# Optimization experiments

Measured on AMD Instinct MI355X. Metric: run time of the kernel, lower is better.

Reference implementation:

```python
import jax, jax.numpy as jnp
import numpy as np

B, P, H, N, D, K = 1024, 1024, 4096, 32, 512, 128


def setup_inputs() -> dict:
    key = jax.random.key(0)
    k1, k2, k3, k4, k5 = jax.random.split(key, 5)
    return {
        "proximal_input": jax.random.normal(k1, (B, P), dtype=jnp.float32),
        "distal_input": jax.random.normal(k2, (B, D), dtype=jnp.float32),
        "W": jax.random.normal(k3, (H, P), dtype=jnp.float32) / np.sqrt(P),
        "b": jax.random.normal(k4, (H,), dtype=jnp.float32) / np.sqrt(P),
        "distal": jax.random.normal(k5, (H, N, D), dtype=jnp.float32),
        "k": K,
    }


def reference(proximal_input, distal_input, W, b, distal, k):
    # proximal path: standard linear -> (B, H)
    proximal_output = proximal_input @ W.T + b
    # per-hidden-unit dendrite projections -> (H, B, N)
    distal_output = jnp.einsum('bd,hnd->hbn', distal_input, distal)
    # pick dominant dendrite by absolute value, keep its signed value
    abs_max_idx = jnp.argmax(jnp.abs(distal_output), axis=-1)          # (H, B)
    distal_max = jnp.take_along_axis(
        distal_output, abs_max_idx[..., None], axis=-1)[..., 0].T      # (B, H)
    # sigmoid gate modulates proximal activations
    result = proximal_output * jax.nn.sigmoid(distal_max)              # (B, H)
    # keep only top-k per row (scatter-built 0/1 mask, as in the original)
    _, top_idxs = jax.lax.top_k(result, k)                             # (B, k)
    rows = jnp.arange(result.shape[0])[:, None]
    mask = jnp.zeros_like(result).at[rows, top_idxs].set(1.0)
    return result * mask
```

## Files before the change

### kernel.cpp

```cpp
#include <hip/hip_runtime.h>
#include <cstdint>
#include <cmath>

#define Bsz  1024
#define Pdim 1024
#define Hdim 4096
#define Ndim 32
#define Ddim 512
#define Ktop 128

typedef _Float16 f16x8  __attribute__((ext_vector_type(8)));
typedef float    f32x16 __attribute__((ext_vector_type(16)));

#define GLDS(gsrc, ldst)                                                        \
  __builtin_amdgcn_global_load_lds(                                             \
      (const __attribute__((address_space(1))) unsigned int*)(gsrc),            \
      (__attribute__((address_space(3))) unsigned int*)(ldst), 16, 0, 0)

#define WS_SERIAL 270532608ull
#define OFF_DIN   268435456ull
#define OFF_W     270532608ull
#define OFF_PIN   287309824ull
#define OFF_GATE  291504128ull
#define WS_FUSED  308281344ull

__global__ __launch_bounds__(256) void convert_img(
    const float* __restrict__ src, char* __restrict__ dst, int kcbits)
{
  const int gid  = blockIdx.x * 256 + threadIdx.x;
  const int row  = gid >> kcbits;
  const int e    = (gid & ((1 << kcbits) - 1)) * 8;
  const int Krow = 8 << kcbits;
  float4 v0 = *(const float4*)(src + (size_t)row * Krow + e);
  float4 v1 = *(const float4*)(src + (size_t)row * Krow + e + 4);
  const int tile = row >> 7, r = row & 127, ks = e >> 5, k = e & 31;
  char* base = dst + (size_t)(tile * (Krow >> 5) + ks) * 16384;
  const int off = ((r >> 5) * 2 + (k >> 4)) * 1024
                + ((r & 31) + 32 * ((k >> 3) & 1)) * 16;
  const float f[8] = {v0.x, v0.y, v0.z, v0.w, v1.x, v1.y, v1.z, v1.w};
  f16x8 hi, lo;
#pragma unroll
  for (int j = 0; j < 8; j++) {
    const _Float16 h = (_Float16)f[j];
    hi[j] = h;
    lo[j] = (_Float16)((f[j] - (float)h) * 256.f);
  }
  *(f16x8*)(base + off)        = hi;
  *(f16x8*)(base + 8192 + off) = lo;
}

template <int NH>
__device__ __forceinline__ void pipe_gemm(
    char (*lds)[16384], const char* Abase, const char* Bbase,
    int lane16, int wv, int wr, int wc,
    f32x16 acc[2][2], f32x16 accx[2][2])
{
  auto STAGE = [&](int h) {
    const int ks = h >> 1, kk = h & 1;
    char* buf = lds[h & 3];
    const char* Ai = Abase + (size_t)ks * 16384;
    const char* Bi = Bbase + (size_t)ks * 16384;
    const char* srcs[4] = {Ai, Ai + 8192, Bi, Bi + 8192};
#pragma unroll
    for (int j = 0; j < 4; j++) {
      const int c = j * 4 + wv;
      GLDS(srcs[j] + (wv * 2 + kk) * 1024 + lane16, buf + c * 1024);
    }
  };

  STAGE(0);
  STAGE(1);
  asm volatile("s_waitcnt vmcnt(4)" ::: "memory");
  __builtin_amdgcn_s_barrier();
  __builtin_amdgcn_sched_barrier(0);

  for (int h = 0; h < NH; ++h) {
    const char* buf = lds[h & 3];
    f16x8 ah[2], al[2], bh[2], bl[2];
#pragma unroll
    for (int mi = 0; mi < 2; mi++) {
      const int m = wr * 2 + mi;
      ah[mi] = *(const f16x8*)(buf + m * 1024 + lane16);
      al[mi] = *(const f16x8*)(buf + 4096 + m * 1024 + lane16);
    }
#pragma unroll
    for (int ni = 0; ni < 2; ni++) {
      const int m = wc * 2 + ni;
      bh[ni] = *(const f16x8*)(buf + 8192 + m * 1024 + lane16);
      bl[ni] = *(const f16x8*)(buf + 12288 + m * 1024 + lane16);
    }
    __builtin_amdgcn_sched_barrier(0);
    if (h + 2 < NH) STAGE(h + 2);
    __builtin_amdgcn_s_barrier();
    __builtin_amdgcn_sched_barrier(0);
    __builtin_amdgcn_s_setprio(1);
#pragma unroll
    for (int ni = 0; ni < 2; ni++)
#pragma unroll
      for (int mi = 0; mi < 2; mi++) {
        acc[mi][ni]  = __builtin_amdgcn_mfma_f32_32x32x16_f16(ah[mi], bh[ni], acc[mi][ni],  0, 0, 0);
        accx[mi][ni] = __builtin_amdgcn_mfma_f32_32x32x16_f16(ah[mi], bl[ni], accx[mi][ni], 0, 0, 0);
        accx[mi][ni] = __builtin_amdgcn_mfma_f32_32x32x16_f16(al[mi], bh[ni], accx[mi][ni], 0, 0, 0);
      }
    __builtin_amdgcn_s_setprio(0);
    if (h + 2 < NH) {
      asm volatile("s_waitcnt vmcnt(4)" ::: "memory");
    } else if (h + 1 < NH) {
      asm volatile("s_waitcnt vmcnt(0)" ::: "memory");
    }
    if (h + 1 < NH) {
      __builtin_amdgcn_s_barrier();
      __builtin_amdgcn_sched_barrier(0);
    }
  }
}

__device__ __forceinline__ void epi_prox(
    f32x16 acc[2][2], f32x16 accx[2][2], const float* bias, float* out,
    int h0, int b0, int wr, int wc, int hi32, int c31)
{
#pragma unroll
  for (int mi = 0; mi < 2; ++mi)
#pragma unroll
    for (int ni = 0; ni < 2; ++ni) {
      const int bcol = b0 + wc * 64 + ni * 32 + c31;
#pragma unroll
      for (int qq = 0; qq < 4; ++qq) {
        const int hb = h0 + wr * 64 + mi * 32 + qq * 8 + hi32 * 4;
        const float4 bb = *(const float4*)(bias + hb);
        float4 o;
        o.x = acc[mi][ni][4*qq+0] + accx[mi][ni][4*qq+0] * 0.00390625f + bb.x;
        o.y = acc[mi][ni][4*qq+1] + accx[mi][ni][4*qq+1] * 0.00390625f + bb.y;
        o.z = acc[mi][ni][4*qq+2] + accx[mi][ni][4*qq+2] * 0.00390625f + bb.z;
        o.w = acc[mi][ni][4*qq+3] + accx[mi][ni][4*qq+3] * 0.00390625f + bb.w;
        *(float4*)(out + (size_t)bcol * Hdim + hb) = o;
      }
    }
}

__device__ __forceinline__ void epi_distal(
    f32x16 acc[2][2], f32x16 accx[2][2], float* out, float* gates,
    int ntile, int btile, int wr, int wc, int hi32, int c31)
{
#pragma unroll
  for (int mi = 0; mi < 2; ++mi)
#pragma unroll
    for (int ni = 0; ni < 2; ++ni) {
      float bestA = -1.f, bestV = 0.f;
      int   bestN = 999;
#pragma unroll
      for (int reg = 0; reg < 16; ++reg) {
        const float v = acc[mi][ni][reg] + accx[mi][ni][reg] * 0.00390625f;
        const float a = fabsf(v);
        const int   n = (reg & 3) + 8 * (reg >> 2) + 4 * hi32;
        if (a > bestA) { bestA = a; bestV = v; bestN = n; }
      }
      {
        const float oa = __shfl_xor(bestA, 32, 64);
        const float ov = __shfl_xor(bestV, 32, 64);
        const int   on = __shfl_xor(bestN, 32, 64);
        if (oa > bestA || (oa == bestA && on < bestN)) {
          bestA = oa; bestV = ov; bestN = on;
        }
      }
      if (hi32 == 0) {
        const int bcol = btile * 128 + wc * 64 + ni * 32 + c31;
        const int h    = ntile * 4 + wr * 2 + mi;
        const float gate = 1.f / (1.f + expf(-bestV));
        const size_t idx = (size_t)bcol * Hdim + h;
        if (gates) gates[idx] = gate;
        else       out[idx] *= gate;
      }
    }
}

__global__ __launch_bounds__(256, 2) void fused_mfma(
    const char* __restrict__ Wimg, const char* __restrict__ Pimg,
    const float* __restrict__ bias, float* __restrict__ out,
    const char* __restrict__ Dimg, const char* __restrict__ Nimg,
    float* __restrict__ gates)
{
  __shared__ __align__(16) char lds[4][16384];
  const int t = threadIdx.x, lane = t & 63, wv = t >> 6;
  const int lane16 = lane * 16;
  const int hi32 = lane >> 5, c31 = lane & 31;
  const int wr = wv >> 1, wc = wv & 1;

  f32x16 acc[2][2], accx[2][2];
#pragma unroll
  for (int mi = 0; mi < 2; mi++)
#pragma unroll
    for (int ni = 0; ni < 2; ni++) {
      acc[mi][ni]  = (f32x16)(0.f);
      accx[mi][ni] = (f32x16)(0.f);
    }

  if (blockIdx.x < 256) {
    const int blk = blockIdx.x;
    const int xcd = blk & 7, q = blk >> 3;
    const int htile = xcd * 4 + (q >> 3);
    const int btile = q & 7;
    pipe_gemm<64>(lds, Wimg + (size_t)(htile * 32) * 16384,
                  Pimg + (size_t)(btile * 32) * 16384,
                  lane16, wv, wr, wc, acc, accx);
    epi_prox(acc, accx, bias, out, htile * 128, btile * 128, wr, wc, hi32, c31);
  } else {
    const int blk = blockIdx.x - 256;
    const int xcd = blk & 7, q = blk >> 3;
    const int ntile = xcd * 128 + (q >> 3);
    const int btile = q & 7;
    pipe_gemm<32>(lds, Dimg + (size_t)(ntile * 16) * 16384,
                  Nimg + (size_t)(btile * 16) * 16384,
                  lane16, wv, wr, wc, acc, accx);
    epi_distal(acc, accx, out, gates, ntile, btile, wr, wc, hi32, c31);
  }
}

__global__ __launch_bounds__(256, 2) void proximal_mfma(
    const char* __restrict__ Aw, const char* __restrict__ Bw,
    const float* __restrict__ bias, float* __restrict__ out)
{
  __shared__ __align__(16) char lds[4][16384];
  const int t = threadIdx.x, lane = t & 63, wv = t >> 6;
  const int lane16 = lane * 16;
  const int hi32 = lane >> 5, c31 = lane & 31;
  const int wr = wv >> 1, wc = wv & 1;
  const int blk = blockIdx.x;
  const int xcd = blk & 7, q = blk >> 3;
  const int htile = xcd * 4 + (q >> 3);
  const int btile = q & 7;

  f32x16 acc[2][2], accx[2][2];
#pragma unroll
  for (int mi = 0; mi < 2; mi++)
#pragma unroll
    for (int ni = 0; ni < 2; ni++) {
      acc[mi][ni]  = (f32x16)(0.f);
      accx[mi][ni] = (f32x16)(0.f);
    }
  pipe_gemm<64>(lds, Aw + (size_t)(htile * 32) * 16384,
                Bw + (size_t)(btile * 32) * 16384,
                lane16, wv, wr, wc, acc, accx);
  epi_prox(acc, accx, bias, out, htile * 128, btile * 128, wr, wc, hi32, c31);
}

__global__ __launch_bounds__(256, 2) void distal_mfma(
    const char* __restrict__ Aw, const char* __restrict__ Bw,
    float* __restrict__ out)
{
  __shared__ __align__(16) char lds[4][16384];
  const int t = threadIdx.x, lane = t & 63, wv = t >> 6;
  const int lane16 = lane * 16;
  const int hi32 = lane >> 5, c31 = lane & 31;
  const int wr = wv >> 1, wc = wv & 1;
  const int blk = blockIdx.x;
  const int xcd = blk & 7, q = blk >> 3;
  const int ntile = xcd * 128 + (q >> 3);
  const int btile = q & 7;

  f32x16 acc[2][2], accx[2][2];
#pragma unroll
  for (int mi = 0; mi < 2; mi++)
#pragma unroll
    for (int ni = 0; ni < 2; ni++) {
      acc[mi][ni]  = (f32x16)(0.f);
      accx[mi][ni] = (f32x16)(0.f);
    }
  pipe_gemm<32>(lds, Aw + (size_t)(ntile * 16) * 16384,
                Bw + (size_t)(btile * 16) * 16384,
                lane16, wv, wr, wc, acc, accx);
  epi_distal(acc, accx, out, nullptr, ntile, btile, wr, wc, hi32, c31);
}

__global__ __launch_bounds__(256) void proximal_gemm(
    const float* __restrict__ pin, const float* __restrict__ W,
    const float* __restrict__ bias, float* __restrict__ out)
{
  __shared__ float Blds[32 * 256];
  __shared__ float Alds[32 * 32];
  const int t  = threadIdx.x;
  const int l  = t & 63;
  const int wv = t >> 6;
  const int ell   = blockIdx.x;
  const int xcd   = ell & 7;
  const int q     = ell >> 3;
  const int htile = xcd * 2 + (q >> 5);
  const int btile = q & 31;
  const int h0 = htile * 256, b0 = btile * 32;

  float acc[8][4];
#pragma unroll
  for (int i = 0; i < 8; i++)
    for (int j = 0; j < 4; j++) acc[i][j] = 0.f;

  const float* wrow = W + (size_t)(h0 + t) * Pdim;
  const int ab = t >> 3, ak = (t & 7) * 4;
  const float* arow = pin + (size_t)(b0 + ab) * Pdim + ak;

  for (int kt = 0; kt < Pdim / 32; ++kt) {
    const int p0 = kt * 32;
    float wbuf[32];
#pragma unroll
    for (int f = 0; f < 8; f++) {
      float4 v = *(const float4*)(wrow + p0 + f * 4);
      wbuf[f * 4 + 0] = v.x; wbuf[f * 4 + 1] = v.y;
      wbuf[f * 4 + 2] = v.z; wbuf[f * 4 + 3] = v.w;
    }
    float4 av = *(const float4*)(arow + p0);
    __syncthreads();
#pragma unroll
    for (int f = 0; f < 32; f++) Blds[f * 256 + t] = wbuf[f];
    Alds[(ak + 0) * 32 + ab] = av.x;
    Alds[(ak + 1) * 32 + ab] = av.y;
    Alds[(ak + 2) * 32 + ab] = av.z;
    Alds[(ak + 3) * 32 + ab] = av.w;
    __syncthreads();
#pragma unroll
    for (int k = 0; k < 32; k++) {
      float4 bv  = *(const float4*)&Blds[k * 256 + 4 * l];
      float4 alo = *(const float4*)&Alds[k * 32 + 8 * wv];
      float4 ahi = *(const float4*)&Alds[k * 32 + 8 * wv + 4];
      float a0[8] = {alo.x, alo.y, alo.z, alo.w, ahi.x, ahi.y, ahi.z, ahi.w};
#pragma unroll
      for (int i = 0; i < 8; i++) {
        acc[i][0] += a0[i] * bv.x;
        acc[i][1] += a0[i] * bv.y;
        acc[i][2] += a0[i] * bv.z;
        acc[i][3] += a0[i] * bv.w;
      }
    }
  }
  float4 bb = *(const float4*)(bias + h0 + 4 * l);
#pragma unroll
  for (int i = 0; i < 8; i++) {
    float4 o;
    o.x = acc[i][0] + bb.x;
    o.y = acc[i][1] + bb.y;
    o.z = acc[i][2] + bb.z;
    o.w = acc[i][3] + bb.w;
    *(float4*)(out + (size_t)(b0 + 8 * wv + i) * Hdim + h0 + 4 * l) = o;
  }
}

__global__ __launch_bounds__(256) void distal_gate_fb(
    const float* __restrict__ din, const float* __restrict__ distal,
    float* __restrict__ out)
{
  __shared__ float Blds[32 * 256];
  __shared__ float Alds[32 * 32];
  const int t  = threadIdx.x;
  const int l  = t & 63;
  const int wv = t >> 6;
  const int ell   = blockIdx.x;
  const int xcd   = ell & 7;
  const int q     = ell >> 3;
  const int htile = xcd * 64 + (q >> 5);
  const int btile = q & 31;
  const int n0 = htile * 256, b0 = btile * 32;

  float acc[8][4];
#pragma unroll
  for (int i = 0; i < 8; i++)
    for (int j = 0; j < 4; j++) acc[i][j] = 0.f;

  const float* brow = distal + (size_t)(n0 + t) * Ddim;
  const int ab = t >> 3, ak = (t & 7) * 4;
  const float* arow = din + (size_t)(b0 + ab) * Ddim + ak;

  for (int kt = 0; kt < Ddim / 32; ++kt) {
    const int d0 = kt * 32;
    float wbuf[32];
#pragma unroll
    for (int f = 0; f < 8; f++) {
      float4 v = *(const float4*)(brow + d0 + f * 4);
      wbuf[f * 4 + 0] = v.x; wbuf[f * 4 + 1] = v.y;
      wbuf[f * 4 + 2] = v.z; wbuf[f * 4 + 3] = v.w;
    }
    float4 av = *(const float4*)(arow + d0);
    __syncthreads();
#pragma unroll
    for (int f = 0; f < 32; f++) Blds[f * 256 + t] = wbuf[f];
    Alds[(ak + 0) * 32 + ab] = av.x;
    Alds[(ak + 1) * 32 + ab] = av.y;
    Alds[(ak + 2) * 32 + ab] = av.z;
    Alds[(ak + 3) * 32 + ab] = av.w;
    __syncthreads();
#pragma unroll
    for (int k = 0; k < 32; k++) {
      float4 bv  = *(const float4*)&Blds[k * 256 + 4 * l];
      float4 alo = *(const float4*)&Alds[k * 32 + 8 * wv];
      float4 ahi = *(const float4*)&Alds[k * 32 + 8 * wv + 4];
      float a0[8] = {alo.x, alo.y, alo.z, alo.w, ahi.x, ahi.y, ahi.z, ahi.w};
#pragma unroll
      for (int i = 0; i < 8; i++) {
        acc[i][0] += a0[i] * bv.x;
        acc[i][1] += a0[i] * bv.y;
        acc[i][2] += a0[i] * bv.z;
        acc[i][3] += a0[i] * bv.w;
      }
    }
  }
  const int i0  = l & 7;
  const int grp = l >> 3;
  float v = 0.f;
#pragma unroll
  for (int bi = 0; bi < 8; bi++) {
    float bav = fabsf(acc[bi][0]);
    float bv_ = acc[bi][0];
    int   bn  = 4 * i0;
#pragma unroll
    for (int j = 1; j < 4; j++) {
      float av2 = fabsf(acc[bi][j]);
      if (av2 > bav) { bav = av2; bv_ = acc[bi][j]; bn = 4 * i0 + j; }
    }
#pragma unroll
    for (int m = 1; m < 8; m <<= 1) {
      float oav = __shfl_xor(bav, m, 64);
      float ov  = __shfl_xor(bv_, m, 64);
      int   on  = __shfl_xor(bn,  m, 64);
      if (oav > bav || (oav == bav && on < bn)) { bav = oav; bv_ = ov; bn = on; }
    }
    if (bi == i0) v = bv_;
  }
  const float gate = 1.f / (1.f + expf(-v));
  const size_t idx = (size_t)(b0 + 8 * wv + i0) * Hdim + (size_t)htile * 8 + grp;
  out[idx] *= gate;
}

__device__ __forceinline__ unsigned keyf(float f) {
  unsigned u = __float_as_uint(f);
  return (u & 0x80000000u) ? ~u : (u | 0x80000000u);
}

__global__ __launch_bounds__(256) void topk_mask(
    float* __restrict__ out, const float* __restrict__ gates)
{
  __shared__ float vals[Hdim];
  __shared__ unsigned hist[256];
  __shared__ unsigned sc[4];
  __shared__ unsigned s_prefix, s_kk;
  const int t = threadIdx.x;
  float* row = out + (size_t)blockIdx.x * Hdim;
  const float* grow = gates ? gates + (size_t)blockIdx.x * Hdim : nullptr;

#pragma unroll
  for (int qq = 0; qq < 4; qq++) {
    float4 v = *(const float4*)(row + qq * 1024 + t * 4);
    if (grow) {
      float4 g = *(const float4*)(grow + qq * 1024 + t * 4);
      v.x *= g.x; v.y *= g.y; v.z *= g.z; v.w *= g.w;
    }
    *(float4*)&vals[qq * 1024 + t * 4] = v;
  }
  if (t == 0) { s_prefix = 0u; s_kk = Ktop; }
  __syncthreads();

  for (int shift = 24; shift >= 0; shift -= 8) {
    hist[t] = 0u;
    __syncthreads();
    const unsigned prefix = s_prefix;
    const unsigned maskhi = (shift == 24) ? 0u : (0xFFFFFFFFu << (shift + 8));
    for (int c = 0; c < 16; c++) {
      unsigned u = keyf(vals[c * 256 + t]);
      if ((u & maskhi) == prefix)
        atomicAdd(&hist[(u >> shift) & 255u], 1u);
    }
    __syncthreads();
    if (t == 0) {
      unsigned kk = s_kk, cum = 0;
      int bin = 255;
      for (; bin > 0; --bin) {
        unsigned c = hist[bin];
        if (cum + c >= kk) break;
        cum += c;
      }
      s_kk = kk - cum;
      s_prefix = prefix | ((unsigned)bin << shift);
    }
    __syncthreads();
  }
  const unsigned T  = s_prefix;
  const unsigned kk = s_kk;

  const int lane = t & 63, w = t >> 6;
  unsigned running = 0;
  for (int c = 0; c < 16; c++) {
    const int h = c * 256 + t;
    const float v = vals[h];
    const unsigned u = keyf(v);
    const bool tie = (u == T);
    unsigned long long m = __ballot(tie);
    unsigned lpfx = (unsigned)__popcll(m & ((1ull << lane) - 1ull));
    if (lane == 0) sc[w] = (unsigned)__popcll(m);
    __syncthreads();
    unsigned off = 0;
#pragma unroll
    for (int ww = 0; ww < 4; ww++) if (ww < w) off += sc[ww];
    const unsigned rank = running + off + lpfx;
    row[h] = (u > T) ? v : ((tie && rank < kk) ? v : 0.f);
    const unsigned tot = sc[0] + sc[1] + sc[2] + sc[3];
    __syncthreads();
    running += tot;
  }
}

extern "C" void kernel_launch(void* const* d_in, const int* in_sizes, int n_in,
                              void* d_out, int out_size, void* d_ws, size_t ws_size,
                              hipStream_t stream)
{
  (void)in_sizes; (void)n_in; (void)out_size;
  const float* pin  = (const float*)d_in[0];
  const float* dinp = (const float*)d_in[1];
  const float* W    = (const float*)d_in[2];
  const float* bias = (const float*)d_in[3];
  const float* dst  = (const float*)d_in[4];
  float* out = (float*)d_out;

  char* ws = (char*)d_ws;
  if (ws_size >= WS_FUSED) {
    hipLaunchKernelGGL(convert_img, dim3(32768), dim3(256), 0, stream, dst,  ws,            6);
    hipLaunchKernelGGL(convert_img, dim3(256),   dim3(256), 0, stream, dinp, ws + OFF_DIN,  6);
    hipLaunchKernelGGL(convert_img, dim3(2048),  dim3(256), 0, stream, W,    ws + OFF_W,    7);
    hipLaunchKernelGGL(convert_img, dim3(512),   dim3(256), 0, stream, pin,  ws + OFF_PIN,  7);
    hipLaunchKernelGGL(fused_mfma,  dim3(8448),  dim3(256), 0, stream,
                       ws + OFF_W, ws + OFF_PIN, bias, out,
                       ws, ws + OFF_DIN, (float*)(ws + OFF_GATE));
    hipLaunchKernelGGL(topk_mask,   dim3(Bsz),   dim3(256), 0, stream, out,
                       (const float*)(ws + OFF_GATE));
  } else if (ws_size >= WS_SERIAL) {
    hipLaunchKernelGGL(convert_img,   dim3(2048),  dim3(256), 0, stream, W,   ws,            7);
    hipLaunchKernelGGL(convert_img,   dim3(512),   dim3(256), 0, stream, pin, ws + 16777216, 7);
    hipLaunchKernelGGL(proximal_mfma, dim3(256),   dim3(256), 0, stream, ws, ws + 16777216, bias, out);
    hipLaunchKernelGGL(convert_img,   dim3(32768), dim3(256), 0, stream, dst,  ws,           6);
    hipLaunchKernelGGL(convert_img,   dim3(256),   dim3(256), 0, stream, dinp, ws + OFF_DIN, 6);
    hipLaunchKernelGGL(distal_mfma,   dim3(8192),  dim3(256), 0, stream, ws, ws + OFF_DIN, out);
    hipLaunchKernelGGL(topk_mask,     dim3(Bsz),   dim3(256), 0, stream, out, (const float*)nullptr);
  } else {
    hipLaunchKernelGGL(proximal_gemm,  dim3(512),   dim3(256), 0, stream, pin, W, bias, out);
    hipLaunchKernelGGL(distal_gate_fb, dim3(16384), dim3(256), 0, stream, dinp, dst, out);
    hipLaunchKernelGGL(topk_mask,      dim3(Bsz),   dim3(256), 0, stream, out, (const float*)nullptr);
  }
}
```

Baseline: 601.7 us.

## Double-buffer MFMA fragments in registers and deepen LDS prefetch to three stages

Restructures the GEMM main loop so the LDS fragments for step h+1 are read into a second register set while MFMAs for step h run. Global-to-LDS prefetch distance grows from two to three stages within the 4-slot ring. It also drops one barrier per iteration. The aim is to hide LDS read latency and global load latency behind the matrix ops, at the cost of more VGPRs and a possible ring-slot hazard, since the stage for h+3 is issued before the reads of h+1 have been fenced by a barrier. The loop assumes NH is even.

```diff
diff --git a/kernel.cpp b/kernel.cpp
--- a/kernel.cpp
+++ b/kernel.cpp
@@ -49,6 +49,45 @@
   *(f16x8*)(base + 8192 + off) = lo;
 }
 
+#define LOADF(F, H)                                                          \
+  { const char* buf_ = lds[(H) & 3];                                         \
+    F[0] = *(const f16x8*)(buf_ +         (wr * 2 + 0) * 1024 + lane16);     \
+    F[1] = *(const f16x8*)(buf_ +         (wr * 2 + 1) * 1024 + lane16);     \
+    F[2] = *(const f16x8*)(buf_ +  4096 + (wr * 2 + 0) * 1024 + lane16);     \
+    F[3] = *(const f16x8*)(buf_ +  4096 + (wr * 2 + 1) * 1024 + lane16);     \
+    F[4] = *(const f16x8*)(buf_ +  8192 + (wc * 2 + 0) * 1024 + lane16);     \
+    F[5] = *(const f16x8*)(buf_ +  8192 + (wc * 2 + 1) * 1024 + lane16);     \
+    F[6] = *(const f16x8*)(buf_ + 12288 + (wc * 2 + 0) * 1024 + lane16);     \
+    F[7] = *(const f16x8*)(buf_ + 12288 + (wc * 2 + 1) * 1024 + lane16); }
+
+#define MFMAC(F)                                                             \
+  __builtin_amdgcn_s_setprio(1);                                             \
+  _Pragma("unroll")                                                          \
+  for (int ni = 0; ni < 2; ni++)                                             \
+    _Pragma("unroll")                                                        \
+    for (int mi = 0; mi < 2; mi++) {                                         \
+      acc[mi][ni]  = __builtin_amdgcn_mfma_f32_32x32x16_f16(F[mi],     F[4 + ni], acc[mi][ni],  0, 0, 0); \
+      accx[mi][ni] = __builtin_amdgcn_mfma_f32_32x32x16_f16(F[mi],     F[6 + ni], accx[mi][ni], 0, 0, 0); \
+      accx[mi][ni] = __builtin_amdgcn_mfma_f32_32x32x16_f16(F[2 + mi], F[4 + ni], accx[mi][ni], 0, 0, 0); \
+    }                                                                        \
+  __builtin_amdgcn_s_setprio(0);
+
+#define WINDOW(H, Fcur, Fnext)                                               \
+  if ((H) + 1 < NH) { LOADF(Fnext, (H) + 1) }                                \
+  __builtin_amdgcn_sched_barrier(0);                                         \
+  if ((H) + 3 < NH) STAGE((H) + 3);                                          \
+  __builtin_amdgcn_sched_barrier(0);                                         \
+  MFMAC(Fcur)                                                                \
+  if ((H) + 1 < NH) {                                                        \
+    if ((H) + 3 < NH) {                                                      \
+      asm volatile("s_waitcnt vmcnt(4)" ::: "memory");                       \
+    } else if ((H) + 2 < NH) {                                               \
+      asm volatile("s_waitcnt vmcnt(0)" ::: "memory");                       \
+    }                                                                        \
+    __builtin_amdgcn_s_barrier();                                            \
+    __builtin_amdgcn_sched_barrier(0);                                       \
+  }
+
 template <int NH>
 __device__ __forceinline__ void pipe_gemm(
     char (*lds)[16384], const char* Abase, const char* Bbase,
@@ -68,50 +107,18 @@
     }
   };
 
-  STAGE(0);
-  STAGE(1);
+  f16x8 fr0[8], fr1[8];
+
+  STAGE(0); STAGE(1); STAGE(2);
   asm volatile("s_waitcnt vmcnt(4)" ::: "memory");
   __builtin_amdgcn_s_barrier();
   __builtin_amdgcn_sched_barrier(0);
-
-  for (int h = 0; h < NH; ++h) {
-    const char* buf = lds[h & 3];
-    f16x8 ah[2], al[2], bh[2], bl[2];
-#pragma unroll
-    for (int mi = 0; mi < 2; mi++) {
-      const int m = wr * 2 + mi;
-      ah[mi] = *(const f16x8*)(buf + m * 1024 + lane16);
-      al[mi] = *(const f16x8*)(buf + 4096 + m * 1024 + lane16);
-    }
-#pragma unroll
-    for (int ni = 0; ni < 2; ni++) {
-      const int m = wc * 2 + ni;
-      bh[ni] = *(const f16x8*)(buf + 8192 + m * 1024 + lane16);
-      bl[ni] = *(const f16x8*)(buf + 12288 + m * 1024 + lane16);
-    }
-    __builtin_amdgcn_sched_barrier(0);
-    if (h + 2 < NH) STAGE(h + 2);
-    __builtin_amdgcn_s_barrier();
-    __builtin_amdgcn_sched_barrier(0);
-    __builtin_amdgcn_s_setprio(1);
-#pragma unroll
-    for (int ni = 0; ni < 2; ni++)
-#pragma unroll
-      for (int mi = 0; mi < 2; mi++) {
-        acc[mi][ni]  = __builtin_amdgcn_mfma_f32_32x32x16_f16(ah[mi], bh[ni], acc[mi][ni],  0, 0, 0);
-        accx[mi][ni] = __builtin_amdgcn_mfma_f32_32x32x16_f16(ah[mi], bl[ni], accx[mi][ni], 0, 0, 0);
-        accx[mi][ni] = __builtin_amdgcn_mfma_f32_32x32x16_f16(al[mi], bh[ni], accx[mi][ni], 0, 0, 0);
-      }
-    __builtin_amdgcn_s_setprio(0);
-    if (h + 2 < NH) {
-      asm volatile("s_waitcnt vmcnt(4)" ::: "memory");
-    } else if (h + 1 < NH) {
-      asm volatile("s_waitcnt vmcnt(0)" ::: "memory");
-    }
-    if (h + 1 < NH) {
-      __builtin_amdgcn_s_barrier();
-      __builtin_amdgcn_sched_barrier(0);
-    }
+  LOADF(fr0, 0)
+  __builtin_amdgcn_sched_barrier(0);
+
+  for (int h = 0; h < NH; h += 2) {
+    WINDOW(h,     fr0, fr1)
+    WINDOW(h + 1, fr1, fr0)
   }
 }
 
```

Result: no change. 605.9 us (+0.7%).
